# Optimization experiments

Hardware: AMD Instinct MI355X
Metric: run time of the kernel (lower is better)

Reference implementation:

```python
import jax, jax.numpy as jnp
import numpy as np

LEVEL = 3  # init kwarg: level=3, wavelet_type='db1' (Haar)


def _haar_step(x):
    """One db1/Haar 2x2 stride-2 decomposition on [B,C,H,W].
    conv2d with kernels outer(l,l),outer(l,h),outer(h,l),outer(h,h), l=h=1/sqrt(2),
    reduces to block sum/difference arithmetic with factor 0.5.
    Returns [B, 4*C, H/2, W/2] in the torch code's channel-major layout
    (c0_LL, c0_LH, c0_HL, c0_HH, c1_LL, ...).
    """
    a = x[..., 0::2, 0::2]
    b = x[..., 0::2, 1::2]
    c = x[..., 1::2, 0::2]
    d = x[..., 1::2, 1::2]
    ll = (a + b + c + d) * 0.5
    lh = (a - b + c - d) * 0.5  # low rows x high cols (cross-correlation)
    hl = (a + b - c - d) * 0.5
    hh = (a - b - c + d) * 0.5
    w = jnp.stack([ll, lh, hl, hh], axis=2)  # [B, C, 4, H/2, W/2]
    B, C = x.shape[0], x.shape[1]
    return w.reshape(B, 4 * C, w.shape[3], w.shape[4])


def setup_inputs() -> dict:
    key = jax.random.key(0)
    x = jax.random.normal(key, (4, 32, 512, 512), dtype=jnp.float32)
    return {"x": x}


def reference(x):
    C = x.shape[1]
    current = x
    highs = []
    for _ in range(LEVEL):
        cur4 = _haar_step(current)        # [B, 4C, h, w]
        low = cur4[:, :C]                 # first C of interleaved subband channels (as in torch code)
        highs.append(cur4[:, C:])         # remaining 3C channels
        current = low
    # torch returns (low, [h1, h2, h3, low])
    return (low, highs[0], highs[1], highs[2], low)
```

## Files before the change

kernel.cpp:

```cpp
#include <hip/hip_runtime.h>


typedef float f4 __attribute__((ext_vector_type(4)));
typedef float f2 __attribute__((ext_vector_type(2)));

#define HAAR(a, b_, c_, d, o0, o1, o2, o3)       \
    o0 = (a + b_ + c_ + d) * 0.5f;               \
    o1 = (a - b_ + c_ - d) * 0.5f;               \
    o2 = (a + b_ - c_ - d) * 0.5f;               \
    o3 = (a - b_ - c_ + d) * 0.5f;

__global__ __launch_bounds__(256) void haar3_fused(
    const float* __restrict__ x,
    float* __restrict__ high1,
    float* __restrict__ high2,
    float* __restrict__ high3,
    float* __restrict__ low3a,
    float* __restrict__ low3b)
{
    const int tid   = threadIdx.x;
    const int tx    = tid & 63;
    const int ty    = tid >> 6;
    const int tileY = blockIdx.x;
    const int bc    = blockIdx.y;
    const int c     = bc & 31;
    const int b     = bc >> 5;

    float w1[4][4][4];
    {
        const float* base = x + ((size_t)bc * 512 + (size_t)(tileY * 32 + ty * 8)) * 512
                              + (size_t)tx * 8;
        #pragma unroll
        for (int i = 0; i < 4; ++i) {
            f4 r0a = *(const f4*)(base + (size_t)(2 * i) * 512);
            f4 r0b = *(const f4*)(base + (size_t)(2 * i) * 512 + 4);
            f4 r1a = *(const f4*)(base + (size_t)(2 * i + 1) * 512);
            f4 r1b = *(const f4*)(base + (size_t)(2 * i + 1) * 512 + 4);
            HAAR(r0a.x, r0a.y, r1a.x, r1a.y, w1[0][i][0], w1[1][i][0], w1[2][i][0], w1[3][i][0]);
            HAAR(r0a.z, r0a.w, r1a.z, r1a.w, w1[0][i][1], w1[1][i][1], w1[2][i][1], w1[3][i][1]);
            HAAR(r0b.x, r0b.y, r1b.x, r1b.y, w1[0][i][2], w1[1][i][2], w1[2][i][2], w1[3][i][2]);
            HAAR(r0b.z, r0b.w, r1b.z, r1b.w, w1[0][i][3], w1[1][i][3], w1[2][i][3], w1[3][i][3]);
        }
    }

    if (c >= 8) {
        float* hp = high1 + ((size_t)b * 96 + (size_t)(4 * (c - 8))) * (256 * 256)
                          + (size_t)(tileY * 16 + ty * 4) * 256 + (size_t)tx * 4;
        #pragma unroll
        for (int s = 0; s < 4; ++s)
            #pragma unroll
            for (int i = 0; i < 4; ++i) {
                f4 v = {w1[s][i][0], w1[s][i][1], w1[s][i][2], w1[s][i][3]};
                __builtin_nontemporal_store(v, (f4*)(hp + (size_t)s * (256 * 256) + i * 256));
            }
        return;
    }

    float w2[16][2][2];
    #pragma unroll
    for (int s = 0; s < 4; ++s)
        #pragma unroll
        for (int i = 0; i < 2; ++i)
            #pragma unroll
            for (int j = 0; j < 2; ++j) {
                float a  = w1[s][2 * i][2 * j];
                float bb = w1[s][2 * i][2 * j + 1];
                float cc = w1[s][2 * i + 1][2 * j];
                float dd = w1[s][2 * i + 1][2 * j + 1];
                HAAR(a, bb, cc, dd, w2[4 * s + 0][i][j], w2[4 * s + 1][i][j],
                                    w2[4 * s + 2][i][j], w2[4 * s + 3][i][j]);
            }

    if (c >= 2) {
        float* hp = high2 + ((size_t)b * 96 + (size_t)(16 * (c - 2))) * (128 * 128)
                          + (size_t)(tileY * 8 + ty * 2) * 128 + (size_t)tx * 2;
        #pragma unroll
        for (int j2 = 0; j2 < 16; ++j2)
            #pragma unroll
            for (int i = 0; i < 2; ++i) {
                f2 v = {w2[j2][i][0], w2[j2][i][1]};
                __builtin_nontemporal_store(v, (f2*)(hp + (size_t)j2 * (128 * 128) + i * 128));
            }
        return;
    }

    const size_t p3  = 64 * 64;
    const size_t sp3 = (size_t)(tileY * 4 + ty) * 64 + (size_t)tx;
    #pragma unroll
    for (int j2 = 0; j2 < 16; ++j2) {
        float a  = w2[j2][0][0];
        float bb = w2[j2][0][1];
        float cc = w2[j2][1][0];
        float dd = w2[j2][1][1];
        float v0, v1, v2, v3;
        HAAR(a, bb, cc, dd, v0, v1, v2, v3);
        float v[4] = {v0, v1, v2, v3};
        #pragma unroll
        for (int s3 = 0; s3 < 4; ++s3) {
            int ch = 64 * c + 4 * j2 + s3;
            if (ch < 32) {
                __builtin_nontemporal_store(v[s3], low3a + ((size_t)b * 32 + ch) * p3 + sp3);
                __builtin_nontemporal_store(v[s3], low3b + ((size_t)b * 32 + ch) * p3 + sp3);
            } else {
                __builtin_nontemporal_store(v[s3], high3 + ((size_t)b * 96 + (ch - 32)) * p3 + sp3);
            }
        }
    }
}

extern "C" void kernel_launch(void* const* d_in, const int* in_sizes, int n_in,
                              void* d_out, int out_size, void* d_ws, size_t ws_size,
                              hipStream_t stream) {
    const float* x = (const float*)d_in[0];
    float* out = (float*)d_out;

    const size_t n_low3  = (size_t)4 * 32 * 64 * 64;
    const size_t n_high1 = (size_t)4 * 96 * 256 * 256;
    const size_t n_high2 = (size_t)4 * 96 * 128 * 128;
    const size_t n_high3 = (size_t)4 * 96 * 64 * 64;

    float* low3a = out;
    float* high1 = out + n_low3;
    float* high2 = high1 + n_high1;
    float* high3 = high2 + n_high2;
    float* low3b = high3 + n_high3;

    dim3 grid(16, 128);
    haar3_fused<<<grid, 256, 0, stream>>>(x, high1, high2, high3, low3a, low3b);
}
```

Measured before the change: 234.0 us.

## Split level-1 high-band channels into a separate fine-grained kernel

The 24 channels that only produce level-1 high bands move into their own kernel, where each thread handles a 2x4 input patch, giving many more blocks and threads for that bandwidth-bound part. The remaining 8 channels per batch keep the fused three-level path in a smaller kernel. This removes divergence inside the fused kernel and gives the dominant traffic more parallelism. The cost is a second launch, narrower stores (f2 instead of f4), and a small second kernel that may underfill the GPU.

```diff
diff --git a/kernel.cpp b/kernel.cpp
--- a/kernel.cpp
+++ b/kernel.cpp
@@ -10,9 +10,36 @@
     o2 = (a + b_ - c_ - d) * 0.5f;               \
     o3 = (a - b_ - c_ + d) * 0.5f;
 
-__global__ __launch_bounds__(256) void haar3_fused(
+__global__ __launch_bounds__(256) void haar_l1_high(
     const float* __restrict__ x,
-    float* __restrict__ high1,
+    float* __restrict__ high1)
+{
+    const int tid = threadIdx.x;
+    const int ow2 = tid & 127;
+    const int oh  = (blockIdx.x << 1) | (tid >> 7);
+    const int bc  = blockIdx.y;
+    const int c24 = bc % 24;
+    const int b   = bc / 24;
+
+    const float* rowbase = x + ((size_t)(b * 32 + c24 + 8) * 512 + (size_t)(2 * oh)) * 512
+                             + (size_t)(4 * ow2);
+    f4 r0 = *(const f4*)(rowbase);
+    f4 r1 = *(const f4*)(rowbase + 512);
+
+    f2 ll, lh, hl, hh;
+    HAAR(r0.x, r0.y, r1.x, r1.y, ll.x, lh.x, hl.x, hh.x);
+    HAAR(r0.z, r0.w, r1.z, r1.w, ll.y, lh.y, hl.y, hh.y);
+
+    float* hp = high1 + ((size_t)b * 96 + (size_t)(4 * c24)) * (256 * 256)
+                      + (size_t)oh * 256 + (size_t)(2 * ow2);
+    __builtin_nontemporal_store(ll, (f2*)(hp));
+    __builtin_nontemporal_store(lh, (f2*)(hp + 1 * 256 * 256));
+    __builtin_nontemporal_store(hl, (f2*)(hp + 2 * 256 * 256));
+    __builtin_nontemporal_store(hh, (f2*)(hp + 3 * 256 * 256));
+}
+
+__global__ __launch_bounds__(256) void haar3_low(
+    const float* __restrict__ x,
     float* __restrict__ high2,
     float* __restrict__ high3,
     float* __restrict__ low3a,
@@ -23,12 +50,12 @@
     const int ty    = tid >> 6;
     const int tileY = blockIdx.x;
     const int bc    = blockIdx.y;
-    const int c     = bc & 31;
-    const int b     = bc >> 5;
+    const int c     = bc & 7;
+    const int b     = bc >> 3;
 
     float w1[4][4][4];
     {
-        const float* base = x + ((size_t)bc * 512 + (size_t)(tileY * 32 + ty * 8)) * 512
+        const float* base = x + ((size_t)(b * 32 + c) * 512 + (size_t)(tileY * 32 + ty * 8)) * 512
                               + (size_t)tx * 8;
         #pragma unroll
         for (int i = 0; i < 4; ++i) {
@@ -41,19 +68,6 @@
             HAAR(r0b.x, r0b.y, r1b.x, r1b.y, w1[0][i][2], w1[1][i][2], w1[2][i][2], w1[3][i][2]);
             HAAR(r0b.z, r0b.w, r1b.z, r1b.w, w1[0][i][3], w1[1][i][3], w1[2][i][3], w1[3][i][3]);
         }
-    }
-
-    if (c >= 8) {
-        float* hp = high1 + ((size_t)b * 96 + (size_t)(4 * (c - 8))) * (256 * 256)
-                          + (size_t)(tileY * 16 + ty * 4) * 256 + (size_t)tx * 4;
-        #pragma unroll
-        for (int s = 0; s < 4; ++s)
-            #pragma unroll
-            for (int i = 0; i < 4; ++i) {
-                f4 v = {w1[s][i][0], w1[s][i][1], w1[s][i][2], w1[s][i][3]};
-                __builtin_nontemporal_store(v, (f4*)(hp + (size_t)s * (256 * 256) + i * 256));
-            }
-        return;
     }
 
     float w2[16][2][2];
@@ -125,6 +139,6 @@
     float* high3 = high2 + n_high2;
     float* low3b = high3 + n_high3;
 
-    dim3 grid(16, 128);
-    haar3_fused<<<grid, 256, 0, stream>>>(x, high1, high2, high3, low3a, low3b);
+    haar_l1_high<<<dim3(128, 96), 256, 0, stream>>>(x, high1);
+    haar3_low<<<dim3(16, 32), 256, 0, stream>>>(x, high2, high3, low3a, low3b);
 }
```

After: 231.6 us. No clear change (-1.0%).

## Split level-1-only channels into a separate finer-grained block path

Applied to the files above, without the earlier changes.

Channels 8..31 need only the first Haar level, so they now get their own block path in which each thread handles one output row pair of 16 input columns, using twice as many blocks (grid 32x128). The multi-level channels keep the old tile path on a separate range of blocks. Loads are also switched to nontemporal. The aim is more parallelism and less work per thread for the bandwidth-bound bulk, with better load balance. The trade-off is half of the multi-level blocks exiting immediately, plus possible changes in coalescing.

```diff
diff --git a/kernel.cpp b/kernel.cpp
--- a/kernel.cpp
+++ b/kernel.cpp
@@ -10,7 +10,7 @@
     o2 = (a + b_ - c_ - d) * 0.5f;               \
     o3 = (a - b_ - c_ + d) * 0.5f;
 
-__global__ __launch_bounds__(256) void haar3_fused(
+__global__ __launch_bounds__(256) void haar_all(
     const float* __restrict__ x,
     float* __restrict__ high1,
     float* __restrict__ high2,
@@ -18,42 +18,71 @@
     float* __restrict__ low3a,
     float* __restrict__ low3b)
 {
-    const int tid   = threadIdx.x;
+    const int tid = threadIdx.x;
+    const int by  = blockIdx.y;
+
+    if (by < 96) {
+        const int c24 = by % 24;
+        const int b   = by / 24;
+        const int oh  = (blockIdx.x << 3) | (tid >> 5);
+        const int oc8 = tid & 31;
+
+        const float* base = x + ((size_t)(b * 32 + c24 + 8) * 512 + (size_t)(2 * oh)) * 512
+                              + (size_t)(16 * oc8);
+        f4 r0[4], r1[4];
+        #pragma unroll
+        for (int q = 0; q < 4; ++q)
+            r0[q] = __builtin_nontemporal_load((const f4*)(base + 4 * q));
+        #pragma unroll
+        for (int q = 0; q < 4; ++q)
+            r1[q] = __builtin_nontemporal_load((const f4*)(base + 512 + 4 * q));
+
+        float LL[8], LH[8], HL[8], HH[8];
+        #pragma unroll
+        for (int q = 0; q < 4; ++q) {
+            HAAR(r0[q].x, r0[q].y, r1[q].x, r1[q].y,
+                 LL[2 * q], LH[2 * q], HL[2 * q], HH[2 * q]);
+            HAAR(r0[q].z, r0[q].w, r1[q].z, r1[q].w,
+                 LL[2 * q + 1], LH[2 * q + 1], HL[2 * q + 1], HH[2 * q + 1]);
+        }
+
+        float* hp = high1 + ((size_t)b * 96 + (size_t)(4 * c24)) * (256 * 256)
+                          + (size_t)oh * 256 + (size_t)(8 * oc8);
+        f4 v;
+        v = (f4){LL[0], LL[1], LL[2], LL[3]};  __builtin_nontemporal_store(v, (f4*)(hp + 0 * 65536));
+        v = (f4){LL[4], LL[5], LL[6], LL[7]};  __builtin_nontemporal_store(v, (f4*)(hp + 0 * 65536 + 4));
+        v = (f4){LH[0], LH[1], LH[2], LH[3]};  __builtin_nontemporal_store(v, (f4*)(hp + 1 * 65536));
+        v = (f4){LH[4], LH[5], LH[6], LH[7]};  __builtin_nontemporal_store(v, (f4*)(hp + 1 * 65536 + 4));
+        v = (f4){HL[0], HL[1], HL[2], HL[3]};  __builtin_nontemporal_store(v, (f4*)(hp + 2 * 65536));
+        v = (f4){HL[4], HL[5], HL[6], HL[7]};  __builtin_nontemporal_store(v, (f4*)(hp + 2 * 65536 + 4));
+        v = (f4){HH[0], HH[1], HH[2], HH[3]};  __builtin_nontemporal_store(v, (f4*)(hp + 3 * 65536));
+        v = (f4){HH[4], HH[5], HH[6], HH[7]};  __builtin_nontemporal_store(v, (f4*)(hp + 3 * 65536 + 4));
+        return;
+    }
+
+    if (blockIdx.x >= 16) return;
+    const int bc    = by - 96;
+    const int c     = bc & 7;
+    const int b     = bc >> 3;
     const int tx    = tid & 63;
     const int ty    = tid >> 6;
     const int tileY = blockIdx.x;
-    const int bc    = blockIdx.y;
-    const int c     = bc & 31;
-    const int b     = bc >> 5;
 
     float w1[4][4][4];
     {
-        const float* base = x + ((size_t)bc * 512 + (size_t)(tileY * 32 + ty * 8)) * 512
+        const float* base = x + ((size_t)(b * 32 + c) * 512 + (size_t)(tileY * 32 + ty * 8)) * 512
                               + (size_t)tx * 8;
         #pragma unroll
         for (int i = 0; i < 4; ++i) {
-            f4 r0a = *(const f4*)(base + (size_t)(2 * i) * 512);
-            f4 r0b = *(const f4*)(base + (size_t)(2 * i) * 512 + 4);
-            f4 r1a = *(const f4*)(base + (size_t)(2 * i + 1) * 512);
-            f4 r1b = *(const f4*)(base + (size_t)(2 * i + 1) * 512 + 4);
+            f4 r0a = __builtin_nontemporal_load((const f4*)(base + (size_t)(2 * i) * 512));
+            f4 r0b = __builtin_nontemporal_load((const f4*)(base + (size_t)(2 * i) * 512 + 4));
+            f4 r1a = __builtin_nontemporal_load((const f4*)(base + (size_t)(2 * i + 1) * 512));
+            f4 r1b = __builtin_nontemporal_load((const f4*)(base + (size_t)(2 * i + 1) * 512 + 4));
             HAAR(r0a.x, r0a.y, r1a.x, r1a.y, w1[0][i][0], w1[1][i][0], w1[2][i][0], w1[3][i][0]);
             HAAR(r0a.z, r0a.w, r1a.z, r1a.w, w1[0][i][1], w1[1][i][1], w1[2][i][1], w1[3][i][1]);
             HAAR(r0b.x, r0b.y, r1b.x, r1b.y, w1[0][i][2], w1[1][i][2], w1[2][i][2], w1[3][i][2]);
             HAAR(r0b.z, r0b.w, r1b.z, r1b.w, w1[0][i][3], w1[1][i][3], w1[2][i][3], w1[3][i][3]);
         }
-    }
-
-    if (c >= 8) {
-        float* hp = high1 + ((size_t)b * 96 + (size_t)(4 * (c - 8))) * (256 * 256)
-                          + (size_t)(tileY * 16 + ty * 4) * 256 + (size_t)tx * 4;
-        #pragma unroll
-        for (int s = 0; s < 4; ++s)
-            #pragma unroll
-            for (int i = 0; i < 4; ++i) {
-                f4 v = {w1[s][i][0], w1[s][i][1], w1[s][i][2], w1[s][i][3]};
-                __builtin_nontemporal_store(v, (f4*)(hp + (size_t)s * (256 * 256) + i * 256));
-            }
-        return;
     }
 
     float w2[16][2][2];
@@ -125,6 +154,5 @@
     float* high3 = high2 + n_high2;
     float* low3b = high3 + n_high3;
 
-    dim3 grid(16, 128);
-    haar3_fused<<<grid, 256, 0, stream>>>(x, high1, high2, high3, low3a, low3b);
+    haar_all<<<dim3(32, 128), 256, 0, stream>>>(x, high1, high2, high3, low3a, low3b);
 }
```

Result: slower. 241.3 us (+3.2%).
